# Optimization experiments

Measured on AMD Instinct MI355X. Metric: run time of the kernel, lower is better.

## Reference

```python
import jax, jax.numpy as jnp
import numpy as np

B, S, K, D = 128, 64, 10, 256
THR = -1.5


def setup_inputs() -> dict:
    key = jax.random.key(0)
    ks = jax.random.split(key, 9)
    si = 1.0 / np.sqrt(D)  # torch GRU init: U(-1/sqrt(hidden), 1/sqrt(hidden))
    u = lambda k, shape, s: jax.random.uniform(k, shape, jnp.float32, -s, s)
    return {
        "item_embs": jax.random.normal(ks[0], (B, S, K, D), jnp.float32),
        "user_embs": jax.random.normal(ks[1], (B, S, D), jnp.float32),
        "W_ih": u(ks[2], (3 * D, 2 * D), si),
        "W_hh": u(ks[3], (3 * D, D), si),
        "b_ih": u(ks[4], (3 * D,), si),
        "b_hh": u(ks[5], (3 * D,), si),
        "w_out": u(ks[6], (D,), si),
        "b_out": u(ks[7], (), si),
        "length": jax.random.randint(ks[8], (B,), 0, S),
    }


def reference(item_embs, user_embs, W_ih, W_hh, b_ih, b_hh, w_out, b_out, length):
    N = B * S
    # x['items'] = cat([item_embs.flatten(0,1), zeros_like(...)], -1)  -> [N, K, 2D]
    items_flat = item_embs.reshape(N, K, D)
    items = jnp.concatenate([items_flat, jnp.zeros_like(items_flat)], axis=-1)
    # user hidden state: gather user_embs at (length-1, clamped), repeat over S
    idx = jnp.clip(length - 1, 0, None)  # [B]
    u0 = user_embs[jnp.arange(B), idx]   # [B, D]
    h0 = jnp.repeat(u0, S, axis=0)       # [N, D]

    def gru_cell(x, h):
        gi = x @ W_ih.T + b_ih  # [N, 3D]
        gh = h @ W_hh.T + b_hh
        i_r, i_z, i_n = jnp.split(gi, 3, axis=-1)
        h_r, h_z, h_n = jnp.split(gh, 3, axis=-1)
        r = jax.nn.sigmoid(i_r + h_r)
        z = jax.nn.sigmoid(i_z + h_z)
        n = jnp.tanh(i_n + r * h_n)
        return (1.0 - z) * n + z * h

    def step(carry, x_t):
        h, mask = carry  # mask [N,1]: readout threshold gate for the click-half of input
        x = jnp.concatenate([x_t[:, :D], x_t[:, D:] * mask], axis=-1)
        h = gru_cell(x, h)
        y = h @ w_out + b_out  # [N]
        next_mask = (jax.lax.stop_gradient(y) > THR).astype(x_t.dtype)[:, None]
        return (h, next_mask), y

    xs = jnp.swapaxes(items, 0, 1)  # [K, N, 2D]
    init = (h0, jnp.ones((N, 1), item_embs.dtype))
    _, ys = jax.lax.scan(step, init, xs)  # ys [K, N]
    y = jnp.swapaxes(ys, 0, 1)  # [N, K]
    # self.w = 1, self.b = 0 -> identity calibration
    return y.reshape(B, S, K)
```

## Files before the change

kernel.cpp:

```cpp
#include <hip/hip_runtime.h>

#define BB 128
#define SS 64
#define KK 10
#define DD 256
#define NN (BB*SS)
#define ROWS 32
#define NBLK (NN/ROWS)
#define NT 1024

typedef __attribute__((ext_vector_type(8))) short short8;
typedef __attribute__((ext_vector_type(4))) float f32x4;
typedef __attribute__((ext_vector_type(4))) unsigned uint4v;

#define FRAG_ELEMS (48*8*64*8)
#define FRAG_ROWS  (48*8*64)

__device__ __forceinline__ unsigned short f2bf(float f){
  union { float f; unsigned u; } v; v.f = f;
  unsigned r = (v.u + 0x7FFFu + ((v.u >> 16) & 1u)) >> 16;
  return (unsigned short)r;
}

__device__ __forceinline__ unsigned cvtpk(float lo, float hi){
  unsigned r;
  asm("v_cvt_pk_bf16_f32 %0, %1, %2" : "=v"(r) : "v"(lo), "v"(hi));
  return r;
}

__global__ void prep_weights(const float* __restrict__ Wih,
                             const float* __restrict__ Whh,
                             unsigned short* __restrict__ fw){
  int t = blockIdx.x * 256 + threadIdx.x;
  int arr = (t >= FRAG_ROWS);
  int r = arr ? (t - FRAG_ROWS) : t;
  int l  = r & 63;
  int tk = (r >> 6) & 7;
  int tn = r >> 9;
  int c  = tn * 16 + (l & 15);
  int d0 = tk * 32 + ((l >> 4) << 3);
  const float* src = arr ? (Whh + (size_t)c*256 + d0) : (Wih + (size_t)c*512 + d0);
  const float4* p = (const float4*)src;
  float4 a0 = p[0], a1 = p[1];
  unsigned short o[8];
  o[0]=f2bf(a0.x); o[1]=f2bf(a0.y); o[2]=f2bf(a0.z); o[3]=f2bf(a0.w);
  o[4]=f2bf(a1.x); o[5]=f2bf(a1.y); o[6]=f2bf(a1.z); o[7]=f2bf(a1.w);
  *(short8*)&fw[(size_t)t*8] = *(short8*)o;
}

__global__ __launch_bounds__(NT, 4) void gru_main(
    const float* __restrict__ item, const float* __restrict__ user,
    const float* __restrict__ b_ih, const float* __restrict__ b_hh,
    const float* __restrict__ w_out, const float* __restrict__ b_out,
    const int* __restrict__ length, const unsigned short* __restrict__ ws,
    float* __restrict__ out)
{
  __shared__ unsigned short xfrag[2][2*8*64*8];
  __shared__ unsigned short hfrag[2][2*8*64*8];
  __shared__ float yp[3][16][2][4][4];

  const int tid  = threadIdx.x;
  const int lane = tid & 63;
  const int w    = tid >> 6;
  const int col  = lane & 15;
  const int q    = lane >> 4;
  const int nb   = blockIdx.x * ROWS;
  const int b    = nb / SS;
  const int sk   = blockIdx.x & 7;

  const short8* fw1 = (const short8*)ws;
  const short8* fwh = fw1 + (FRAG_ELEMS/8);

  const int d    = w*16 + col;
  const float br_  = b_ih[d]       + b_hh[d];
  const float bz_  = b_ih[256 + d] + b_hh[256 + d];
  const float bin_ = b_ih[512 + d];
  const float bhn_ = b_hh[512 + d];
  const float wo_  = w_out[d];

  const int wq0 = (w     )*512 + lane;
  const int wq1 = (16 + w)*512 + lane;
  const int wq2 = (32 + w)*512 + lane;

  int idx = length[b] - 1; if (idx < 0) idx = 0;
  const float u0 = user[((size_t)b*SS + idx)*DD + d];
  float h[2][4];
  #pragma unroll
  for (int mt = 0; mt < 2; ++mt)
    #pragma unroll
    for (int reg = 0; reg < 4; ++reg)
      h[mt][reg] = u0;

  const int tkk = d >> 5;
  const int slb = ((d >> 3) & 3) * 16;
  const int dj  = d & 7;
  {
    unsigned short hb = f2bf(u0);
    #pragma unroll
    for (int mt = 0; mt < 2; ++mt)
      #pragma unroll
      for (int reg = 0; reg < 4; ++reg)
        hfrag[0][((mt*8 + tkk)*64 + slb + q*4 + reg)*8 + dj] = hb;
  }

  const int xrow = tid >> 5;
  const int xo   = tid & 31;
  const int xmt  = xrow >> 4;
  const int xtk  = xo >> 2;
  const int xsl  = (xo & 3)*16 + (xrow & 15);
  #pragma unroll
  for (int s = 0; s < 2; ++s){
    const float4* p = (const float4*)(item + ((size_t)(nb + xrow)*KK + s)*DD + xo*8);
    float4 a0 = p[0], a1 = p[1];
    uint4v t;
    t.x = cvtpk(a0.x, a0.y); t.y = cvtpk(a0.z, a0.w);
    t.z = cvtpk(a1.x, a1.y); t.w = cvtpk(a1.z, a1.w);
    *(uint4v*)&xfrag[s][((xmt*8 + xtk)*64 + xsl)*8] = t;
  }
  __syncthreads();

  const float bout = b_out[0];

#define MFMA16(A,Bv,C) __builtin_amdgcn_mfma_f32_16x16x32_bf16(A,Bv,C,0,0,0)

  for (int c = 0; c < KK/2; ++c){
    f32x4 gi[2][2][3];
    #pragma unroll
    for (int s = 0; s < 2; ++s)
      #pragma unroll
      for (int mt = 0; mt < 2; ++mt)
        #pragma unroll
        for (int g = 0; g < 3; ++g){
          f32x4 z4 = {0.f, 0.f, 0.f, 0.f};
          gi[s][mt][g] = z4;
        }

    #pragma unroll 2
    for (int tk = 0; tk < 8; ++tk){
      const int tkv = (tk + sk) & 7;
      const int o_  = tkv * 64;
      short8 w1r = fw1[wq0+o_], w1z = fw1[wq1+o_], w1n = fw1[wq2+o_];
      short8 a00 = *(const short8*)&xfrag[0][((    tkv)*64 + lane)*8];
      short8 a01 = *(const short8*)&xfrag[0][((8 + tkv)*64 + lane)*8];
      short8 a10 = *(const short8*)&xfrag[1][((    tkv)*64 + lane)*8];
      short8 a11 = *(const short8*)&xfrag[1][((8 + tkv)*64 + lane)*8];
      __builtin_amdgcn_s_setprio(1);
      gi[0][0][0] = MFMA16(a00, w1r, gi[0][0][0]);
      gi[0][0][1] = MFMA16(a00, w1z, gi[0][0][1]);
      gi[0][0][2] = MFMA16(a00, w1n, gi[0][0][2]);
      gi[0][1][0] = MFMA16(a01, w1r, gi[0][1][0]);
      gi[0][1][1] = MFMA16(a01, w1z, gi[0][1][1]);
      gi[0][1][2] = MFMA16(a01, w1n, gi[0][1][2]);
      gi[1][0][0] = MFMA16(a10, w1r, gi[1][0][0]);
      gi[1][0][1] = MFMA16(a10, w1z, gi[1][0][1]);
      gi[1][0][2] = MFMA16(a10, w1n, gi[1][0][2]);
      gi[1][1][0] = MFMA16(a11, w1r, gi[1][1][0]);
      gi[1][1][1] = MFMA16(a11, w1z, gi[1][1][1]);
      gi[1][1][2] = MFMA16(a11, w1n, gi[1][1][2]);
      __builtin_amdgcn_s_setprio(0);
    }

    #pragma unroll
    for (int s = 0; s < 2; ++s){
      const int k   = 2*c + s;
      const int cb  = s;
      const int nbf = s ^ 1;

      f32x4 acc[2][3];
      #pragma unroll
      for (int mt = 0; mt < 2; ++mt){
        acc[mt][0] = gi[s][mt][0];
        acc[mt][1] = gi[s][mt][1];
        f32x4 z4 = {0.f, 0.f, 0.f, 0.f};
        acc[mt][2] = z4;
      }

      float4 xa0, xa1, xb0, xb1;
      if (s == 1 && c < KK/2-1){
        const float4* pA = (const float4*)(item + ((size_t)(nb + xrow)*KK + (2*c+2))*DD + xo*8);
        const float4* pB = (const float4*)(item + ((size_t)(nb + xrow)*KK + (2*c+3))*DD + xo*8);
        xa0 = pA[0]; xa1 = pA[1]; xb0 = pB[0]; xb1 = pB[1];
      }

      #pragma unroll 4
      for (int tk = 0; tk < 8; ++tk){
        const int tkv = (tk + sk) & 7;
        const int o_  = tkv * 64;
        short8 whr = fwh[wq0+o_], whz = fwh[wq1+o_], whn = fwh[wq2+o_];
        short8 ah0 = *(const short8*)&hfrag[cb][((    tkv)*64 + lane)*8];
        short8 ah1 = *(const short8*)&hfrag[cb][((8 + tkv)*64 + lane)*8];
        __builtin_amdgcn_s_setprio(1);
        acc[0][0] = MFMA16(ah0, whr, acc[0][0]);
        acc[0][1] = MFMA16(ah0, whz, acc[0][1]);
        acc[0][2] = MFMA16(ah0, whn, acc[0][2]);
        acc[1][0] = MFMA16(ah1, whr, acc[1][0]);
        acc[1][1] = MFMA16(ah1, whz, acc[1][1]);
        acc[1][2] = MFMA16(ah1, whn, acc[1][2]);
        __builtin_amdgcn_s_setprio(0);
      }

      float ypl[2][4];
      #pragma unroll
      for (int mt = 0; mt < 2; ++mt)
        #pragma unroll
        for (int reg = 0; reg < 4; ++reg){
          float rp = acc[mt][0][reg] + br_;
          float zp = acc[mt][1][reg] + bz_;
          float r  = __builtin_amdgcn_rcpf(1.f + __expf(-rp));
          float z  = __builtin_amdgcn_rcpf(1.f + __expf(-zp));
          float np = gi[s][mt][2][reg] + bin_ + r*(acc[mt][2][reg] + bhn_);
          np = __builtin_amdgcn_fmed3f(np, -30.f, 30.f);
          float e  = __expf(2.f*np);
          float n  = 1.f - 2.f*__builtin_amdgcn_rcpf(e + 1.f);
          float hv = (1.f - z)*n + z*h[mt][reg];
          h[mt][reg] = hv;
          ypl[mt][reg] = hv * wo_;
        }

      #pragma unroll
      for (int mt = 0; mt < 2; ++mt)
        #pragma unroll
        for (int reg = 0; reg < 4; ++reg){
          float p = ypl[mt][reg];
          p += __shfl_xor(p, 1);
          p += __shfl_xor(p, 2);
          p += __shfl_xor(p, 4);
          p += __shfl_xor(p, 8);
          if (col == 0) yp[k % 3][w][mt][q][reg] = p;
        }

      #pragma unroll
      for (int mt = 0; mt < 2; ++mt)
        #pragma unroll
        for (int reg = 0; reg < 4; ++reg)
          hfrag[nbf][((mt*8 + tkk)*64 + slb + q*4 + reg)*8 + dj] = f2bf(h[mt][reg]);

      if (s == 1 && c < KK/2-1){
        uint4v t;
        t.x = cvtpk(xa0.x, xa0.y); t.y = cvtpk(xa0.z, xa0.w);
        t.z = cvtpk(xa1.x, xa1.y); t.w = cvtpk(xa1.z, xa1.w);
        *(uint4v*)&xfrag[0][((xmt*8 + xtk)*64 + xsl)*8] = t;
        t.x = cvtpk(xb0.x, xb0.y); t.y = cvtpk(xb0.z, xb0.w);
        t.z = cvtpk(xb1.x, xb1.y); t.w = cvtpk(xb1.z, xb1.w);
        *(uint4v*)&xfrag[1][((xmt*8 + xtk)*64 + xsl)*8] = t;
      }

      if (k > 0 && tid < 32){
        float sacc = bout;
        #pragma unroll
        for (int ww = 0; ww < 16; ++ww)
          sacc += yp[(k-1) % 3][ww][tid >> 4][(tid >> 2) & 3][tid & 3];
        out[(size_t)(nb + tid)*KK + (k-1)] = sacc;
      }

      asm volatile("s_waitcnt lgkmcnt(0)" ::: "memory");
      __builtin_amdgcn_s_barrier();
      __builtin_amdgcn_sched_barrier(0);
    }
  }

  if (tid < 32){
    float s = bout;
    #pragma unroll
    for (int ww = 0; ww < 16; ++ww)
      s += yp[(KK-1) % 3][ww][tid >> 4][(tid >> 2) & 3][tid & 3];
    out[(size_t)(nb + tid)*KK + (KK-1)] = s;
  }
}

extern "C" void kernel_launch(void* const* d_in, const int* in_sizes, int n_in,
                              void* d_out, int out_size, void* d_ws, size_t ws_size,
                              hipStream_t stream) {
  const float* item   = (const float*)d_in[0];
  const float* user   = (const float*)d_in[1];
  const float* W_ih   = (const float*)d_in[2];
  const float* W_hh   = (const float*)d_in[3];
  const float* b_ih   = (const float*)d_in[4];
  const float* b_hh   = (const float*)d_in[5];
  const float* w_out  = (const float*)d_in[6];
  const float* b_out  = (const float*)d_in[7];
  const int*   length = (const int*)d_in[8];
  unsigned short* ws  = (unsigned short*)d_ws;
  float* out = (float*)d_out;

  hipLaunchKernelGGL(prep_weights, dim3((2*FRAG_ROWS)/256), dim3(256), 0, stream,
                     W_ih, W_hh, ws);
  hipLaunchKernelGGL(gru_main, dim3(NBLK), dim3(NT), 0, stream,
                     item, user, b_ih, b_hh, w_out, b_out, length, ws, out);
}
```

Baseline: 218.5 us.

## Halve block rows to 16 with 512 threads, each wave covering two column tiles

Changes the per-block tile from 32 rows and 16 waves to 16 rows and 8 waves, so each wave now computes two 16-column output groups (d and d+128) instead of two row tiles. Twice as many blocks are launched, with smaller shared-memory buffers and one A fragment reused against two weight column sets. This raises parallelism across CUs and shortens each block's serial recurrence work. In exchange, total weight-fragment reads from global/L2 double because each block still streams all of W_ih and W_hh for only half the rows.

After: 256.6 us. 1.17x slower.

```diff
diff --git a/kernel.cpp b/kernel.cpp
--- a/kernel.cpp
+++ b/kernel.cpp
@@ -5,9 +5,9 @@
 #define KK 10
 #define DD 256
 #define NN (BB*SS)
-#define ROWS 32
+#define ROWS 16
 #define NBLK (NN/ROWS)
-#define NT 1024
+#define NT 512
 
 typedef __attribute__((ext_vector_type(8))) short short8;
 typedef __attribute__((ext_vector_type(4))) float f32x4;
@@ -55,9 +55,9 @@
     const int* __restrict__ length, const unsigned short* __restrict__ ws,
     float* __restrict__ out)
 {
-  __shared__ unsigned short xfrag[2][2*8*64*8];
-  __shared__ unsigned short hfrag[2][2*8*64*8];
-  __shared__ float yp[3][16][2][4][4];
+  __shared__ unsigned short xfrag[2][8*64*8];
+  __shared__ unsigned short hfrag[2][8*64*8];
+  __shared__ float yp[3][16][4][4];
 
   const int tid  = threadIdx.x;
   const int lane = tid & 63;
@@ -71,43 +71,45 @@
   const short8* fw1 = (const short8*)ws;
   const short8* fwh = fw1 + (FRAG_ELEMS/8);
 
-  const int d    = w*16 + col;
-  const float br_  = b_ih[d]       + b_hh[d];
-  const float bz_  = b_ih[256 + d] + b_hh[256 + d];
-  const float bin_ = b_ih[512 + d];
-  const float bhn_ = b_hh[512 + d];
-  const float wo_  = w_out[d];
+  const int d0 = w*16 + col;
+  const int d1 = d0 + 128;
+  float br_g[2], bz_g[2], bin_g[2], bhn_g[2], wo_g[2];
+  br_g[0]  = b_ih[d0]       + b_hh[d0];       br_g[1]  = b_ih[d1]       + b_hh[d1];
+  bz_g[0]  = b_ih[256 + d0] + b_hh[256 + d0]; bz_g[1]  = b_ih[256 + d1] + b_hh[256 + d1];
+  bin_g[0] = b_ih[512 + d0];                  bin_g[1] = b_ih[512 + d1];
+  bhn_g[0] = b_hh[512 + d0];                  bhn_g[1] = b_hh[512 + d1];
+  wo_g[0]  = w_out[d0];                       wo_g[1]  = w_out[d1];
 
   const int wq0 = (w     )*512 + lane;
   const int wq1 = (16 + w)*512 + lane;
   const int wq2 = (32 + w)*512 + lane;
 
   int idx = length[b] - 1; if (idx < 0) idx = 0;
-  const float u0 = user[((size_t)b*SS + idx)*DD + d];
+  float u0g[2];
+  u0g[0] = user[((size_t)b*SS + idx)*DD + d0];
+  u0g[1] = user[((size_t)b*SS + idx)*DD + d1];
   float h[2][4];
   #pragma unroll
-  for (int mt = 0; mt < 2; ++mt)
+  for (int g = 0; g < 2; ++g)
     #pragma unroll
     for (int reg = 0; reg < 4; ++reg)
-      h[mt][reg] = u0;
-
-  const int tkk = d >> 5;
-  const int slb = ((d >> 3) & 3) * 16;
-  const int dj  = d & 7;
-  {
-    unsigned short hb = f2bf(u0);
-    #pragma unroll
-    for (int mt = 0; mt < 2; ++mt)
-      #pragma unroll
-      for (int reg = 0; reg < 4; ++reg)
-        hfrag[0][((mt*8 + tkk)*64 + slb + q*4 + reg)*8 + dj] = hb;
+      h[g][reg] = u0g[g];
+
+  const int tkk = d0 >> 5;
+  const int slb = ((d0 >> 3) & 3) * 16;
+  const int dj  = d0 & 7;
+  #pragma unroll
+  for (int g = 0; g < 2; ++g){
+    unsigned short hb = f2bf(u0g[g]);
+    #pragma unroll
+    for (int reg = 0; reg < 4; ++reg)
+      hfrag[0][((tkk + 4*g)*64 + slb + q*4 + reg)*8 + dj] = hb;
   }
 
   const int xrow = tid >> 5;
   const int xo   = tid & 31;
-  const int xmt  = xrow >> 4;
   const int xtk  = xo >> 2;
-  const int xsl  = (xo & 3)*16 + (xrow & 15);
+  const int xsl  = (xo & 3)*16 + xrow;
   #pragma unroll
   for (int s = 0; s < 2; ++s){
     const float4* p = (const float4*)(item + ((size_t)(nb + xrow)*KK + s)*DD + xo*8);
@@ -115,7 +117,7 @@
     uint4v t;
     t.x = cvtpk(a0.x, a0.y); t.y = cvtpk(a0.z, a0.w);
     t.z = cvtpk(a1.x, a1.y); t.w = cvtpk(a1.z, a1.w);
-    *(uint4v*)&xfrag[s][((xmt*8 + xtk)*64 + xsl)*8] = t;
+    *(uint4v*)&xfrag[s][((xtk)*64 + xsl)*8] = t;
   }
   __syncthreads();
 
@@ -128,35 +130,34 @@
     #pragma unroll
     for (int s = 0; s < 2; ++s)
       #pragma unroll
-      for (int mt = 0; mt < 2; ++mt)
-        #pragma unroll
-        for (int g = 0; g < 3; ++g){
+      for (int g = 0; g < 2; ++g)
+        #pragma unroll
+        for (int kd = 0; kd < 3; ++kd){
           f32x4 z4 = {0.f, 0.f, 0.f, 0.f};
-          gi[s][mt][g] = z4;
+          gi[s][g][kd] = z4;
         }
 
     #pragma unroll 2
     for (int tk = 0; tk < 8; ++tk){
       const int tkv = (tk + sk) & 7;
       const int o_  = tkv * 64;
-      short8 w1r = fw1[wq0+o_], w1z = fw1[wq1+o_], w1n = fw1[wq2+o_];
-      short8 a00 = *(const short8*)&xfrag[0][((    tkv)*64 + lane)*8];
-      short8 a01 = *(const short8*)&xfrag[0][((8 + tkv)*64 + lane)*8];
-      short8 a10 = *(const short8*)&xfrag[1][((    tkv)*64 + lane)*8];
-      short8 a11 = *(const short8*)&xfrag[1][((8 + tkv)*64 + lane)*8];
+      short8 wr0 = fw1[wq0+o_],      wz0 = fw1[wq1+o_],      wn0 = fw1[wq2+o_];
+      short8 wr1 = fw1[wq0+4096+o_], wz1 = fw1[wq1+4096+o_], wn1 = fw1[wq2+4096+o_];
+      short8 a0 = *(const short8*)&xfrag[0][((tkv)*64 + lane)*8];
+      short8 a1 = *(const short8*)&xfrag[1][((tkv)*64 + lane)*8];
       __builtin_amdgcn_s_setprio(1);
-      gi[0][0][0] = MFMA16(a00, w1r, gi[0][0][0]);
-      gi[0][0][1] = MFMA16(a00, w1z, gi[0][0][1]);
-      gi[0][0][2] = MFMA16(a00, w1n, gi[0][0][2]);
-      gi[0][1][0] = MFMA16(a01, w1r, gi[0][1][0]);
-      gi[0][1][1] = MFMA16(a01, w1z, gi[0][1][1]);
-      gi[0][1][2] = MFMA16(a01, w1n, gi[0][1][2]);
-      gi[1][0][0] = MFMA16(a10, w1r, gi[1][0][0]);
-      gi[1][0][1] = MFMA16(a10, w1z, gi[1][0][1]);
-      gi[1][0][2] = MFMA16(a10, w1n, gi[1][0][2]);
-      gi[1][1][0] = MFMA16(a11, w1r, gi[1][1][0]);
-      gi[1][1][1] = MFMA16(a11, w1z, gi[1][1][1]);
-      gi[1][1][2] = MFMA16(a11, w1n, gi[1][1][2]);
+      gi[0][0][0] = MFMA16(a0, wr0, gi[0][0][0]);
+      gi[0][0][1] = MFMA16(a0, wz0, gi[0][0][1]);
+      gi[0][0][2] = MFMA16(a0, wn0, gi[0][0][2]);
+      gi[0][1][0] = MFMA16(a0, wr1, gi[0][1][0]);
+      gi[0][1][1] = MFMA16(a0, wz1, gi[0][1][1]);
+      gi[0][1][2] = MFMA16(a0, wn1, gi[0][1][2]);
+      gi[1][0][0] = MFMA16(a1, wr0, gi[1][0][0]);
+      gi[1][0][1] = MFMA16(a1, wz0, gi[1][0][1]);
+      gi[1][0][2] = MFMA16(a1, wn0, gi[1][0][2]);
+      gi[1][1][0] = MFMA16(a1, wr1, gi[1][1][0]);
+      gi[1][1][1] = MFMA16(a1, wz1, gi[1][1][1]);
+      gi[1][1][2] = MFMA16(a1, wn1, gi[1][1][2]);
       __builtin_amdgcn_s_setprio(0);
     }
 
@@ -168,11 +169,11 @@
 
       f32x4 acc[2][3];
       #pragma unroll
-      for (int mt = 0; mt < 2; ++mt){
-        acc[mt][0] = gi[s][mt][0];
-        acc[mt][1] = gi[s][mt][1];
+      for (int g = 0; g < 2; ++g){
+        acc[g][0] = gi[s][g][0];
+        acc[g][1] = gi[s][g][1];
         f32x4 z4 = {0.f, 0.f, 0.f, 0.f};
-        acc[mt][2] = z4;
+        acc[g][2] = z4;
       }
 
       float4 xa0, xa1, xb0, xb1;
@@ -182,74 +183,74 @@
         xa0 = pA[0]; xa1 = pA[1]; xb0 = pB[0]; xb1 = pB[1];
       }
 
-      #pragma unroll 4
+      #pragma unroll 2
       for (int tk = 0; tk < 8; ++tk){
         const int tkv = (tk + sk) & 7;
         const int o_  = tkv * 64;
-        short8 whr = fwh[wq0+o_], whz = fwh[wq1+o_], whn = fwh[wq2+o_];
-        short8 ah0 = *(const short8*)&hfrag[cb][((    tkv)*64 + lane)*8];
-        short8 ah1 = *(const short8*)&hfrag[cb][((8 + tkv)*64 + lane)*8];
+        short8 hr0 = fwh[wq0+o_],      hz0 = fwh[wq1+o_],      hn0 = fwh[wq2+o_];
+        short8 hr1 = fwh[wq0+4096+o_], hz1 = fwh[wq1+4096+o_], hn1 = fwh[wq2+4096+o_];
+        short8 ah = *(const short8*)&hfrag[cb][((tkv)*64 + lane)*8];
         __builtin_amdgcn_s_setprio(1);
-        acc[0][0] = MFMA16(ah0, whr, acc[0][0]);
-        acc[0][1] = MFMA16(ah0, whz, acc[0][1]);
-        acc[0][2] = MFMA16(ah0, whn, acc[0][2]);
-        acc[1][0] = MFMA16(ah1, whr, acc[1][0]);
-        acc[1][1] = MFMA16(ah1, whz, acc[1][1]);
-        acc[1][2] = MFMA16(ah1, whn, acc[1][2]);
+        acc[0][0] = MFMA16(ah, hr0, acc[0][0]);
+        acc[0][1] = MFMA16(ah, hz0, acc[0][1]);
+        acc[0][2] = MFMA16(ah, hn0, acc[0][2]);
+        acc[1][0] = MFMA16(ah, hr1, acc[1][0]);
+        acc[1][1] = MFMA16(ah, hz1, acc[1][1]);
+        acc[1][2] = MFMA16(ah, hn1, acc[1][2]);
         __builtin_amdgcn_s_setprio(0);
       }
 
       float ypl[2][4];
       #pragma unroll
-      for (int mt = 0; mt < 2; ++mt)
+      for (int g = 0; g < 2; ++g)
         #pragma unroll
         for (int reg = 0; reg < 4; ++reg){
-          float rp = acc[mt][0][reg] + br_;
-          float zp = acc[mt][1][reg] + bz_;
+          float rp = acc[g][0][reg] + br_g[g];
+          float zp = acc[g][1][reg] + bz_g[g];
           float r  = __builtin_amdgcn_rcpf(1.f + __expf(-rp));
           float z  = __builtin_amdgcn_rcpf(1.f + __expf(-zp));
-          float np = gi[s][mt][2][reg] + bin_ + r*(acc[mt][2][reg] + bhn_);
+          float np = gi[s][g][2][reg] + bin_g[g] + r*(acc[g][2][reg] + bhn_g[g]);
           np = __builtin_amdgcn_fmed3f(np, -30.f, 30.f);
           float e  = __expf(2.f*np);
           float n  = 1.f - 2.f*__builtin_amdgcn_rcpf(e + 1.f);
-          float hv = (1.f - z)*n + z*h[mt][reg];
-          h[mt][reg] = hv;
-          ypl[mt][reg] = hv * wo_;
+          float hv = (1.f - z)*n + z*h[g][reg];
+          h[g][reg] = hv;
+          ypl[g][reg] = hv * wo_g[g];
         }
 
       #pragma unroll
-      for (int mt = 0; mt < 2; ++mt)
+      for (int g = 0; g < 2; ++g)
         #pragma unroll
         for (int reg = 0; reg < 4; ++reg){
-          float p = ypl[mt][reg];
+          float p = ypl[g][reg];
           p += __shfl_xor(p, 1);
           p += __shfl_xor(p, 2);
           p += __shfl_xor(p, 4);
           p += __shfl_xor(p, 8);
-          if (col == 0) yp[k % 3][w][mt][q][reg] = p;
+          if (col == 0) yp[k % 3][w + 8*g][q][reg] = p;
         }
 
       #pragma unroll
-      for (int mt = 0; mt < 2; ++mt)
+      for (int g = 0; g < 2; ++g)
         #pragma unroll
         for (int reg = 0; reg < 4; ++reg)
-          hfrag[nbf][((mt*8 + tkk)*64 + slb + q*4 + reg)*8 + dj] = f2bf(h[mt][reg]);
+          hfrag[nbf][((tkk + 4*g)*64 + slb + q*4 + reg)*8 + dj] = f2bf(h[g][reg]);
 
       if (s == 1 && c < KK/2-1){
         uint4v t;
         t.x = cvtpk(xa0.x, xa0.y); t.y = cvtpk(xa0.z, xa0.w);
         t.z = cvtpk(xa1.x, xa1.y); t.w = cvtpk(xa1.z, xa1.w);
-        *(uint4v*)&xfrag[0][((xmt*8 + xtk)*64 + xsl)*8] = t;
+        *(uint4v*)&xfrag[0][((xtk)*64 + xsl)*8] = t;
         t.x = cvtpk(xb0.x, xb0.y); t.y = cvtpk(xb0.z, xb0.w);
         t.z = cvtpk(xb1.x, xb1.y); t.w = cvtpk(xb1.z, xb1.w);
-        *(uint4v*)&xfrag[1][((xmt*8 + xtk)*64 + xsl)*8] = t;
-      }
-
-      if (k > 0 && tid < 32){
+        *(uint4v*)&xfrag[1][((xtk)*64 + xsl)*8] = t;
+      }
+
+      if (k > 0 && tid < 16){
         float sacc = bout;
         #pragma unroll
         for (int ww = 0; ww < 16; ++ww)
-          sacc += yp[(k-1) % 3][ww][tid >> 4][(tid >> 2) & 3][tid & 3];
+          sacc += yp[(k-1) % 3][ww][tid >> 2][tid & 3];
         out[(size_t)(nb + tid)*KK + (k-1)] = sacc;
       }
 
@@ -259,11 +260,11 @@
     }
   }
 
-  if (tid < 32){
+  if (tid < 16){
     float s = bout;
     #pragma unroll
     for (int ww = 0; ww < 16; ++ww)
-      s += yp[(KK-1) % 3][ww][tid >> 4][(tid >> 2) & 3][tid & 3];
+      s += yp[(KK-1) % 3][ww][tid >> 2][tid & 3];
     out[(size_t)(nb + tid)*KK + (KK-1)] = s;
   }
 }
```

## Halve rows per block to 16 and double grid size

Applied to the files above, without the earlier changes.

Each block now handles 16 rows instead of 32, so each wave does one M-tile per MFMA group instead of two. The grid doubles and launch bounds request 8 blocks per CU, with halved LDS usage per block. The aim is more parallelism and latency hiding across the sequential GRU steps. The cost is that each weight fragment loaded from global/L2 now feeds half as many MFMAs, so total weight traffic doubles.

Result: slower. 281.4 us (+28.8%).

```diff
diff --git a/kernel.cpp b/kernel.cpp
--- a/kernel.cpp
+++ b/kernel.cpp
@@ -5,7 +5,7 @@
 #define KK 10
 #define DD 256
 #define NN (BB*SS)
-#define ROWS 32
+#define ROWS 16
 #define NBLK (NN/ROWS)
 #define NT 1024
 
@@ -48,16 +48,16 @@
   *(short8*)&fw[(size_t)t*8] = *(short8*)o;
 }
 
-__global__ __launch_bounds__(NT, 4) void gru_main(
+__global__ __launch_bounds__(NT, 8) void gru_main(
     const float* __restrict__ item, const float* __restrict__ user,
     const float* __restrict__ b_ih, const float* __restrict__ b_hh,
     const float* __restrict__ w_out, const float* __restrict__ b_out,
     const int* __restrict__ length, const unsigned short* __restrict__ ws,
     float* __restrict__ out)
 {
-  __shared__ unsigned short xfrag[2][2*8*64*8];
-  __shared__ unsigned short hfrag[2][2*8*64*8];
-  __shared__ float yp[3][16][2][4][4];
+  __shared__ unsigned short xfrag[2][8*64*8];
+  __shared__ unsigned short hfrag[2][8*64*8];
+  __shared__ float yp[3][16][4][4];
 
   const int tid  = threadIdx.x;
   const int lane = tid & 63;
@@ -84,12 +84,9 @@
 
   int idx = length[b] - 1; if (idx < 0) idx = 0;
   const float u0 = user[((size_t)b*SS + idx)*DD + d];
-  float h[2][4];
+  float h[4];
   #pragma unroll
-  for (int mt = 0; mt < 2; ++mt)
-    #pragma unroll
-    for (int reg = 0; reg < 4; ++reg)
-      h[mt][reg] = u0;
+  for (int reg = 0; reg < 4; ++reg) h[reg] = u0;
 
   const int tkk = d >> 5;
   const int slb = ((d >> 3) & 3) * 16;
@@ -97,25 +94,22 @@
   {
     unsigned short hb = f2bf(u0);
     #pragma unroll
-    for (int mt = 0; mt < 2; ++mt)
-      #pragma unroll
-      for (int reg = 0; reg < 4; ++reg)
-        hfrag[0][((mt*8 + tkk)*64 + slb + q*4 + reg)*8 + dj] = hb;
-  }
-
-  const int xrow = tid >> 5;
+    for (int reg = 0; reg < 4; ++reg)
+      hfrag[0][((tkk)*64 + slb + q*4 + reg)*8 + dj] = hb;
+  }
+
+  const int xs   = tid >> 9;
+  const int xrow = (tid >> 5) & 15;
   const int xo   = tid & 31;
-  const int xmt  = xrow >> 4;
   const int xtk  = xo >> 2;
-  const int xsl  = (xo & 3)*16 + (xrow & 15);
-  #pragma unroll
-  for (int s = 0; s < 2; ++s){
-    const float4* p = (const float4*)(item + ((size_t)(nb + xrow)*KK + s)*DD + xo*8);
+  const int xsl  = (xo & 3)*16 + xrow;
+  {
+    const float4* p = (const float4*)(item + ((size_t)(nb + xrow)*KK + xs)*DD + xo*8);
     float4 a0 = p[0], a1 = p[1];
     uint4v t;
     t.x = cvtpk(a0.x, a0.y); t.y = cvtpk(a0.z, a0.w);
     t.z = cvtpk(a1.x, a1.y); t.w = cvtpk(a1.z, a1.w);
-    *(uint4v*)&xfrag[s][((xmt*8 + xtk)*64 + xsl)*8] = t;
+    *(uint4v*)&xfrag[xs][((xtk)*64 + xsl)*8] = t;
   }
   __syncthreads();
 
@@ -124,39 +118,29 @@
 #define MFMA16(A,Bv,C) __builtin_amdgcn_mfma_f32_16x16x32_bf16(A,Bv,C,0,0,0)
 
   for (int c = 0; c < KK/2; ++c){
-    f32x4 gi[2][2][3];
+    f32x4 gi[2][3];
     #pragma unroll
     for (int s = 0; s < 2; ++s)
       #pragma unroll
-      for (int mt = 0; mt < 2; ++mt)
-        #pragma unroll
-        for (int g = 0; g < 3; ++g){
-          f32x4 z4 = {0.f, 0.f, 0.f, 0.f};
-          gi[s][mt][g] = z4;
-        }
+      for (int g = 0; g < 3; ++g){
+        f32x4 z4 = {0.f, 0.f, 0.f, 0.f};
+        gi[s][g] = z4;
+      }
 
     #pragma unroll 2
     for (int tk = 0; tk < 8; ++tk){
       const int tkv = (tk + sk) & 7;
       const int o_  = tkv * 64;
       short8 w1r = fw1[wq0+o_], w1z = fw1[wq1+o_], w1n = fw1[wq2+o_];
-      short8 a00 = *(const short8*)&xfrag[0][((    tkv)*64 + lane)*8];
-      short8 a01 = *(const short8*)&xfrag[0][((8 + tkv)*64 + lane)*8];
-      short8 a10 = *(const short8*)&xfrag[1][((    tkv)*64 + lane)*8];
-      short8 a11 = *(const short8*)&xfrag[1][((8 + tkv)*64 + lane)*8];
+      short8 a0 = *(const short8*)&xfrag[0][((tkv)*64 + lane)*8];
+      short8 a1 = *(const short8*)&xfrag[1][((tkv)*64 + lane)*8];
       __builtin_amdgcn_s_setprio(1);
-      gi[0][0][0] = MFMA16(a00, w1r, gi[0][0][0]);
-      gi[0][0][1] = MFMA16(a00, w1z, gi[0][0][1]);
-      gi[0][0][2] = MFMA16(a00, w1n, gi[0][0][2]);
-      gi[0][1][0] = MFMA16(a01, w1r, gi[0][1][0]);
-      gi[0][1][1] = MFMA16(a01, w1z, gi[0][1][1]);
-      gi[0][1][2] = MFMA16(a01, w1n, gi[0][1][2]);
-      gi[1][0][0] = MFMA16(a10, w1r, gi[1][0][0]);
-      gi[1][0][1] = MFMA16(a10, w1z, gi[1][0][1]);
-      gi[1][0][2] = MFMA16(a10, w1n, gi[1][0][2]);
-      gi[1][1][0] = MFMA16(a11, w1r, gi[1][1][0]);
-      gi[1][1][1] = MFMA16(a11, w1z, gi[1][1][1]);
-      gi[1][1][2] = MFMA16(a11, w1n, gi[1][1][2]);
+      gi[0][0] = MFMA16(a0, w1r, gi[0][0]);
+      gi[0][1] = MFMA16(a0, w1z, gi[0][1]);
+      gi[0][2] = MFMA16(a0, w1n, gi[0][2]);
+      gi[1][0] = MFMA16(a1, w1r, gi[1][0]);
+      gi[1][1] = MFMA16(a1, w1z, gi[1][1]);
+      gi[1][2] = MFMA16(a1, w1n, gi[1][2]);
       __builtin_amdgcn_s_setprio(0);
     }
 
@@ -166,20 +150,15 @@
       const int cb  = s;
       const int nbf = s ^ 1;
 
-      f32x4 acc[2][3];
-      #pragma unroll
-      for (int mt = 0; mt < 2; ++mt){
-        acc[mt][0] = gi[s][mt][0];
-        acc[mt][1] = gi[s][mt][1];
-        f32x4 z4 = {0.f, 0.f, 0.f, 0.f};
-        acc[mt][2] = z4;
-      }
-
-      float4 xa0, xa1, xb0, xb1;
+      f32x4 acc[3];
+      acc[0] = gi[s][0];
+      acc[1] = gi[s][1];
+      { f32x4 z4 = {0.f, 0.f, 0.f, 0.f}; acc[2] = z4; }
+
+      float4 xa0, xa1;
       if (s == 1 && c < KK/2-1){
-        const float4* pA = (const float4*)(item + ((size_t)(nb + xrow)*KK + (2*c+2))*DD + xo*8);
-        const float4* pB = (const float4*)(item + ((size_t)(nb + xrow)*KK + (2*c+3))*DD + xo*8);
-        xa0 = pA[0]; xa1 = pA[1]; xb0 = pB[0]; xb1 = pB[1];
+        const float4* p = (const float4*)(item + ((size_t)(nb + xrow)*KK + (2*c+2+xs))*DD + xo*8);
+        xa0 = p[0]; xa1 = p[1];
       }
 
       #pragma unroll 4
@@ -187,69 +166,56 @@
         const int tkv = (tk + sk) & 7;
         const int o_  = tkv * 64;
         short8 whr = fwh[wq0+o_], whz = fwh[wq1+o_], whn = fwh[wq2+o_];
-        short8 ah0 = *(const short8*)&hfrag[cb][((    tkv)*64 + lane)*8];
-        short8 ah1 = *(const short8*)&hfrag[cb][((8 + tkv)*64 + lane)*8];
+        short8 ah = *(const short8*)&hfrag[cb][((tkv)*64 + lane)*8];
         __builtin_amdgcn_s_setprio(1);
-        acc[0][0] = MFMA16(ah0, whr, acc[0][0]);
-        acc[0][1] = MFMA16(ah0, whz, acc[0][1]);
-        acc[0][2] = MFMA16(ah0, whn, acc[0][2]);
-        acc[1][0] = MFMA16(ah1, whr, acc[1][0]);
-        acc[1][1] = MFMA16(ah1, whz, acc[1][1]);
-        acc[1][2] = MFMA16(ah1, whn, acc[1][2]);
+        acc[0] = MFMA16(ah, whr, acc[0]);
+        acc[1] = MFMA16(ah, whz, acc[1]);
+        acc[2] = MFMA16(ah, whn, acc[2]);
         __builtin_amdgcn_s_setprio(0);
       }
 
-      float ypl[2][4];
-      #pragma unroll
-      for (int mt = 0; mt < 2; ++mt)
-        #pragma unroll
-        for (int reg = 0; reg < 4; ++reg){
-          float rp = acc[mt][0][reg] + br_;
-          float zp = acc[mt][1][reg] + bz_;
-          float r  = __builtin_amdgcn_rcpf(1.f + __expf(-rp));
-          float z  = __builtin_amdgcn_rcpf(1.f + __expf(-zp));
-          float np = gi[s][mt][2][reg] + bin_ + r*(acc[mt][2][reg] + bhn_);
-          np = __builtin_amdgcn_fmed3f(np, -30.f, 30.f);
-          float e  = __expf(2.f*np);
-          float n  = 1.f - 2.f*__builtin_amdgcn_rcpf(e + 1.f);
-          float hv = (1.f - z)*n + z*h[mt][reg];
-          h[mt][reg] = hv;
-          ypl[mt][reg] = hv * wo_;
-        }
-
-      #pragma unroll
-      for (int mt = 0; mt < 2; ++mt)
-        #pragma unroll
-        for (int reg = 0; reg < 4; ++reg){
-          float p = ypl[mt][reg];
-          p += __shfl_xor(p, 1);
-          p += __shfl_xor(p, 2);
-          p += __shfl_xor(p, 4);
-          p += __shfl_xor(p, 8);
-          if (col == 0) yp[k % 3][w][mt][q][reg] = p;
-        }
-
-      #pragma unroll
-      for (int mt = 0; mt < 2; ++mt)
-        #pragma unroll
-        for (int reg = 0; reg < 4; ++reg)
-          hfrag[nbf][((mt*8 + tkk)*64 + slb + q*4 + reg)*8 + dj] = f2bf(h[mt][reg]);
+      float ypl[4];
+      #pragma unroll
+      for (int reg = 0; reg < 4; ++reg){
+        float rp = acc[0][reg] + br_;
+        float zp = acc[1][reg] + bz_;
+        float r  = __builtin_amdgcn_rcpf(1.f + __expf(-rp));
+        float z  = __builtin_amdgcn_rcpf(1.f + __expf(-zp));
+        float np = gi[s][2][reg] + bin_ + r*(acc[2][reg] + bhn_);
+        np = __builtin_amdgcn_fmed3f(np, -30.f, 30.f);
+        float e  = __expf(2.f*np);
+        float n  = 1.f - 2.f*__builtin_amdgcn_rcpf(e + 1.f);
+        float hv = (1.f - z)*n + z*h[reg];
+        h[reg] = hv;
+        ypl[reg] = hv * wo_;
+      }
+
+      #pragma unroll
+      for (int reg = 0; reg < 4; ++reg){
+        float p = ypl[reg];
+        p += __shfl_xor(p, 1);
+        p += __shfl_xor(p, 2);
+        p += __shfl_xor(p, 4);
+        p += __shfl_xor(p, 8);
+        if (col == 0) yp[k % 3][w][q][reg] = p;
+      }
+
+      #pragma unroll
+      for (int reg = 0; reg < 4; ++reg)
+        hfrag[nbf][((tkk)*64 + slb + q*4 + reg)*8 + dj] = f2bf(h[reg]);
 
       if (s == 1 && c < KK/2-1){
         uint4v t;
         t.x = cvtpk(xa0.x, xa0.y); t.y = cvtpk(xa0.z, xa0.w);
         t.z = cvtpk(xa1.x, xa1.y); t.w = cvtpk(xa1.z, xa1.w);
-        *(uint4v*)&xfrag[0][((xmt*8 + xtk)*64 + xsl)*8] = t;
-        t.x = cvtpk(xb0.x, xb0.y); t.y = cvtpk(xb0.z, xb0.w);
-        t.z = cvtpk(xb1.x, xb1.y); t.w = cvtpk(xb1.z, xb1.w);
-        *(uint4v*)&xfrag[1][((xmt*8 + xtk)*64 + xsl)*8] = t;
-      }
-
-      if (k > 0 && tid < 32){
+        *(uint4v*)&xfrag[xs][((xtk)*64 + xsl)*8] = t;
+      }
+
+      if (k > 0 && tid < 16){
         float sacc = bout;
         #pragma unroll
         for (int ww = 0; ww < 16; ++ww)
-          sacc += yp[(k-1) % 3][ww][tid >> 4][(tid >> 2) & 3][tid & 3];
+          sacc += yp[(k-1) % 3][ww][tid >> 2][tid & 3];
         out[(size_t)(nb + tid)*KK + (k-1)] = sacc;
       }
 
@@ -259,11 +225,11 @@
     }
   }
 
-  if (tid < 32){
+  if (tid < 16){
     float s = bout;
     #pragma unroll
     for (int ww = 0; ww < 16; ++ww)
-      s += yp[(KK-1) % 3][ww][tid >> 4][(tid >> 2) & 3][tid & 3];
+      s += yp[(KK-1) % 3][ww][tid >> 2][tid & 3];
     out[(size_t)(nb + tid)*KK + (KK-1)] = s;
   }
 }
```
